# Optimization experiments

Hardware: AMD Instinct MI355X
Metric: run time of the kernel (lower is better)

The kernel has to match this reference:

```python
import jax, jax.numpy as jnp
import numpy as np

B, T, D, M = 4, 2048, 512, 8  # batch, seq, d(=d_out), n_head
LN_EPS = 1e-5


def setup_inputs() -> dict:
    key = jax.random.key(0)
    k = jax.random.split(key, 6)
    s = 1.0 / np.sqrt(D)
    x = jax.random.normal(k[0], (B, T, D), jnp.float32)
    P = jax.random.normal(k[1], (M, D, D), jnp.float32) * s
    Q = jax.random.normal(k[2], (M, D, D), jnp.float32) * s
    K = jax.random.normal(k[3], (M, D, D), jnp.float32) * s
    Wo = jax.random.normal(k[4], (D, M * D), jnp.float32) * (1.0 / np.sqrt(M * D))  # (d_out, m*d), torch Linear layout
    bo = jax.random.normal(k[5], (D,), jnp.float32) * 0.01
    gamma = jnp.ones((D,), jnp.float32)
    beta = jnp.zeros((D,), jnp.float32)
    return {"x": x, "P": P, "Q": Q, "K": K, "Wo": Wo, "bo": bo, "gamma": gamma, "beta": beta}


def reference(x, P, Q, K, Wo, bo, gamma, beta):
    b, t, d = x.shape
    m = P.shape[0]
    # per-head projections: (B,T,d) x (m,d,d) -> (B,m,T,d)
    QZ = jnp.einsum('btj,mij->bmti', x, Q)
    KZ = jnp.einsum('btj,mij->bmti', x, K)   # have_key_proj=True
    PZ = jnp.einsum('btj,mij->bmti', x, P)   # value-side projection
    # causal softmax attention
    scores = jnp.einsum('bmti,bmsi->bmts', QZ, KZ) / jnp.sqrt(jnp.asarray(d, x.dtype))
    mask = jnp.tril(jnp.ones((t, t), dtype=bool))  # (T,T) causal
    scores = jnp.where(mask, scores, -jnp.inf)
    attn = jax.nn.softmax(scores, axis=-1)
    out = jnp.einsum('bmts,bmsi->bmti', attn, PZ)
    # have_output_proj=True: concat heads then Linear(m*d -> d_out)
    out = out.transpose(0, 2, 1, 3).reshape(b, t, m * d)
    y = out @ Wo.T + bo
    # layer norm of (attn_out + residual)
    h = y + x
    mu = jnp.mean(h, axis=-1, keepdims=True)
    var = jnp.var(h, axis=-1, keepdims=True)
    return (h - mu) / jnp.sqrt(var + LN_EPS) * gamma + beta
```

## Files before the change

### kernel.cpp

```cpp
#include <hip/hip_runtime.h>

typedef unsigned short u16;
typedef __attribute__((ext_vector_type(8))) short bf16x8;
typedef __attribute__((ext_vector_type(8))) unsigned short u16x8;
typedef __attribute__((ext_vector_type(4))) float f32x4;

__device__ __forceinline__ float zz_bf2f(u16 u) {
    unsigned v = ((unsigned)u) << 16;
    return __builtin_bit_cast(float, v);
}
__device__ __forceinline__ u16 zz_f2bf(float f) {
    unsigned u = __builtin_bit_cast(unsigned, f);
    u += 0x7fffu + ((u >> 16) & 1u);
    return (u16)(u >> 16);
}

__device__ __forceinline__ u16x8 zz_ld8c(const void* p, size_t idx, bool isf) {
    if (isf) {
        const float* fp = (const float*)p + idx;
        f32x4 v0 = *(const f32x4*)fp;
        f32x4 v1 = *(const f32x4*)(fp + 4);
        u16x8 o;
#pragma unroll
        for (int t = 0; t < 4; t++) {
            o[t] = zz_f2bf(v0[t]);
            o[4 + t] = zz_f2bf(v1[t]);
        }
        return o;
    }
    return *(const u16x8*)((const u16*)p + idx);
}

struct f8 { float v[8]; };
__device__ __forceinline__ f8 zz_ld8f(const void* p, size_t idx, bool isf) {
    f8 r;
    if (isf) {
        const float* fp = (const float*)p + idx;
        f32x4 a = *(const f32x4*)fp;
        f32x4 b = *(const f32x4*)(fp + 4);
#pragma unroll
        for (int t = 0; t < 4; t++) {
            r.v[t] = a[t];
            r.v[4 + t] = b[t];
        }
    } else {
        const u16* up = (const u16*)p + idx;
#pragma unroll
        for (int t = 0; t < 8; t++) r.v[t] = zz_bf2f(up[t]);
    }
    return r;
}

__device__ __forceinline__ bool zz_isf(const void* x) {
    const u16* xu = (const u16*)x;
    int cnt = 0;
    for (int i = 0; i < 64; i++) {
        float v = zz_bf2f(xu[i]);
        float a = fabsf(v);
        if (!(a <= 1e8f) || (v != 0.f && a < 1e-8f)) cnt++;
    }
    return cnt >= 16;
}

#define MFMA16(a, b, c) __builtin_amdgcn_mfma_f32_16x16x32_bf16((a), (b), (c), 0, 0, 0)

__device__ __forceinline__ void zz_gll16(const u16* g, u16* l) {
    __builtin_amdgcn_global_load_lds((const __attribute__((address_space(1))) unsigned int*)g,
                                     (__attribute__((address_space(3))) unsigned int*)l, 16, 0, 0);
}

__global__ __launch_bounds__(256) void zk25_conv(const void* __restrict__ x, const void* __restrict__ p1,
                                                 const void* __restrict__ p2, const void* __restrict__ p3,
                                                 const void* __restrict__ p4, u16* __restrict__ xc,
                                                 u16* __restrict__ c1, u16* __restrict__ c2,
                                                 u16* __restrict__ c3, u16* __restrict__ c4) {
    const bool isf = zz_isf(x);
    const int t = blockIdx.y;
    const void* src = (t == 0) ? x : (t == 1) ? p1 : (t == 2) ? p2 : (t == 3) ? p3 : p4;
    u16* dst = (t == 0) ? xc : (t == 1) ? c1 : (t == 2) ? c2 : (t == 3) ? c3 : c4;
    const unsigned n = (t == 0) ? 4194304u : 2097152u;
    const unsigned i = (blockIdx.x * 256u + threadIdx.x) * 8u;
    if (i >= n) return;
    *(u16x8*)(dst + i) = zz_ld8c(src, i, isf);
}

__device__ __forceinline__ void zz_gemm128(const u16* __restrict__ A, size_t aOff,
                                           const u16* __restrict__ B, size_t bOff,
                                           int K, int lda, int ldb, int tm, int tn,
                                           u16* As, u16* Bs, f32x4 acc[4][4]) {
    const int tid = threadIdx.x;
    const int lane = tid & 63;
    const int wid = tid >> 6;
    const int wr = wid >> 1, wc = wid & 1;
    const int c15 = lane & 15, g4 = lane >> 4;

    const int rA = tid >> 2;
    const int cA = (tid & 3) << 3;
    const u16* pA0 = A + aOff + (size_t)(tm * 128 + rA) * lda + cA;
    const u16* pA1 = pA0 + (size_t)64 * lda;
    const u16* pB0 = B + bOff + (size_t)(tn * 128 + rA) * ldb + cA;
    const u16* pB1 = pB0 + (size_t)64 * ldb;
    u16* sA0 = As + tid * 8;
    u16* sA1 = sA0 + 64 * 32;
    u16* sB0 = Bs + tid * 8;
    u16* sB1 = sB0 + 64 * 32;

    for (int k0 = 0; k0 < K; k0 += 32) {
        __syncthreads();
        zz_gll16(pA0 + k0, sA0);
        zz_gll16(pA1 + k0, sA1);
        zz_gll16(pB0 + k0, sB0);
        zz_gll16(pB1 + k0, sB1);
        __syncthreads();
        bf16x8 af[4], bfr[4];
#pragma unroll
        for (int mf = 0; mf < 4; mf++)
            af[mf] = *(const bf16x8*)(As + (wr * 64 + mf * 16 + c15) * 32 + g4 * 8);
#pragma unroll
        for (int nf = 0; nf < 4; nf++)
            bfr[nf] = *(const bf16x8*)(Bs + (wc * 64 + nf * 16 + c15) * 32 + g4 * 8);
#pragma unroll
        for (int mf = 0; mf < 4; mf++)
#pragma unroll
            for (int nf = 0; nf < 4; nf++) acc[mf][nf] = MFMA16(af[mf], bfr[nf], acc[mf][nf]);
    }
}

__global__ __launch_bounds__(256) void zk25_proj(const u16* __restrict__ xc, int b, int g0, int G,
                                                 const u16* __restrict__ Qc, const u16* __restrict__ Kc,
                                                 const u16* __restrict__ Pc,
                                                 u16* __restrict__ QZ, u16* __restrict__ KZ,
                                                 u16* __restrict__ Vt) {
    __shared__ u16 As[128 * 32];
    __shared__ u16 Bs[128 * 32];
    const size_t TD = (size_t)2048 * 512;
    const size_t WD = (size_t)512 * 512;
    const int seg = blockIdx.y;
    const int part = seg / G;
    const int g = seg - part * G;
    const int head = g0 + g;
    const size_t xOff = (size_t)b * TD;
    const int bx = blockIdx.x;

    f32x4 acc[4][4];
    const f32x4 zf = {0.f, 0.f, 0.f, 0.f};
#pragma unroll
    for (int i = 0; i < 4; i++)
#pragma unroll
        for (int j = 0; j < 4; j++) acc[i][j] = zf;

    const int lane = threadIdx.x & 63;
    const int wid = threadIdx.x >> 6;
    const int wr = wid >> 1, wc = wid & 1;
    const int c15 = lane & 15, g4 = lane >> 4;

    if (part < 2) {
        const u16* W = (part == 0) ? Qc : Kc;
        u16* C = ((part == 0) ? QZ : KZ) + (size_t)g * TD;
        const int tm = bx >> 2, tn = bx & 3;
        zz_gemm128(xc, xOff, W, (size_t)head * WD, 512, 512, 512, tm, tn, As, Bs, acc);
#pragma unroll
        for (int mf = 0; mf < 4; mf++)
#pragma unroll
            for (int nf = 0; nf < 4; nf++) {
                const int row0 = tm * 128 + wr * 64 + mf * 16 + g4 * 4;
                const int col = tn * 128 + wc * 64 + nf * 16 + c15;
#pragma unroll
                for (int r = 0; r < 4; r++) C[(size_t)(row0 + r) * 512 + col] = zz_f2bf(acc[mf][nf][r]);
            }
    } else {
        u16* C = Vt + (size_t)g * TD;
        const int tm = bx >> 4, tn = bx & 15;
        zz_gemm128(Pc, (size_t)head * WD, xc, xOff, 512, 512, 512, tm, tn, As, Bs, acc);
#pragma unroll
        for (int mf = 0; mf < 4; mf++)
#pragma unroll
            for (int nf = 0; nf < 4; nf++) {
                const int row0 = tm * 128 + wr * 64 + mf * 16 + g4 * 4;
                const int col = tn * 128 + wc * 64 + nf * 16 + c15;
#pragma unroll
                for (int r = 0; r < 4; r++) C[(size_t)(row0 + r) * 2048 + col] = zz_f2bf(acc[mf][nf][r]);
            }
    }
}

__global__ __launch_bounds__(256) void zk25_qk(const u16* __restrict__ QZ, const u16* __restrict__ KZ,
                                               u16* __restrict__ Sp) {
    const int tm = blockIdx.x, tn = blockIdx.y;
    if (tn > tm) return;
    const int g = blockIdx.z;
    __shared__ u16 As[128 * 32];
    __shared__ u16 Bs[128 * 32];
    const size_t TD = (size_t)2048 * 512;

    f32x4 acc[4][4];
    const f32x4 zf = {0.f, 0.f, 0.f, 0.f};
#pragma unroll
    for (int i = 0; i < 4; i++)
#pragma unroll
        for (int j = 0; j < 4; j++) acc[i][j] = zf;

    zz_gemm128(QZ, (size_t)g * TD, KZ, (size_t)g * TD, 512, 512, 512, tm, tn, As, Bs, acc);

    const int lane = threadIdx.x & 63;
    const int wid = threadIdx.x >> 6;
    const int wr = wid >> 1, wc = wid & 1;
    const int c15 = lane & 15, g4 = lane >> 4;
    u16* Sg = Sp + (size_t)g * 2048 * 2048;
#pragma unroll
    for (int mf = 0; mf < 4; mf++)
#pragma unroll
        for (int nf = 0; nf < 4; nf++) {
            const int row0 = tm * 128 + wr * 64 + mf * 16 + g4 * 4;
            const int col = tn * 128 + wc * 64 + nf * 16 + c15;
#pragma unroll
            for (int r = 0; r < 4; r++) Sg[(size_t)(row0 + r) * 2048 + col] = zz_f2bf(acc[mf][nf][r]);
        }
}

__global__ __launch_bounds__(256) void zk25_sm(u16* __restrict__ Sp) {
    const int g = blockIdx.y;
    const int wid = threadIdx.x >> 6, lane = threadIdx.x & 63;
    const int t = blockIdx.x * 4 + wid;
    u16* rowp = Sp + (size_t)g * 2048 * 2048 + (size_t)t * 2048 + lane * 32;
    const float SCL2 = 0.06375826722338107f;
    u16x8 raw[4];
#pragma unroll
    for (int i = 0; i < 4; i++) raw[i] = *(const u16x8*)(rowp + i * 8);
    float v[32];
    float mx = -INFINITY;
#pragma unroll
    for (int i = 0; i < 32; i++) {
        const int s = lane * 32 + i;
        v[i] = (s <= t) ? zz_bf2f(raw[i >> 3][i & 7]) * SCL2 : -INFINITY;
        mx = fmaxf(mx, v[i]);
    }
#pragma unroll
    for (int d = 1; d < 64; d <<= 1) mx = fmaxf(mx, __shfl_xor(mx, d));
    float p[32];
    float sum = 0.f;
#pragma unroll
    for (int i = 0; i < 32; i++) {
        p[i] = exp2f(v[i] - mx);
        sum += p[i];
    }
#pragma unroll
    for (int d = 1; d < 64; d <<= 1) sum += __shfl_xor(sum, d);
    const float inv = 1.f / sum;
#pragma unroll
    for (int i = 0; i < 4; i++) {
        u16x8 o;
#pragma unroll
        for (int j = 0; j < 8; j++) o[j] = zz_f2bf(p[i * 8 + j] * inv);
        *(u16x8*)(rowp + i * 8) = o;
    }
}

__global__ __launch_bounds__(256) void zk25_pv(const u16* __restrict__ Sp, const u16* __restrict__ Vt,
                                               u16* __restrict__ Oc, int g0) {
    __shared__ u16 As[128 * 32];
    __shared__ u16 Bs[128 * 32];
    const int g = blockIdx.y;
    const int bx = blockIdx.x;
    const int tm = bx >> 2, tn = bx & 3;
    const int K = (tm + 1) * 128;
    const size_t TD = (size_t)2048 * 512;

    f32x4 acc[4][4];
    const f32x4 zf = {0.f, 0.f, 0.f, 0.f};
#pragma unroll
    for (int i = 0; i < 4; i++)
#pragma unroll
        for (int j = 0; j < 4; j++) acc[i][j] = zf;

    zz_gemm128(Sp, (size_t)g * 2048 * 2048, Vt, (size_t)g * TD, K, 2048, 2048, tm, tn, As, Bs, acc);

    const int lane = threadIdx.x & 63;
    const int wid = threadIdx.x >> 6;
    const int wr = wid >> 1, wc = wid & 1;
    const int c15 = lane & 15, g4 = lane >> 4;
    u16* Ob = Oc + (size_t)(g0 + g) * 512;
#pragma unroll
    for (int mf = 0; mf < 4; mf++)
#pragma unroll
        for (int nf = 0; nf < 4; nf++) {
            const int row0 = tm * 128 + wr * 64 + mf * 16 + g4 * 4;
            const int col = tn * 128 + wc * 64 + nf * 16 + c15;
#pragma unroll
            for (int r = 0; r < 4; r++) Ob[(size_t)(row0 + r) * 4096 + col] = zz_f2bf(acc[mf][nf][r]);
        }
}

__global__ __launch_bounds__(256) void zk25_oproj(const u16* __restrict__ Oc, const u16* __restrict__ Woc,
                                                  float* __restrict__ y4) {
    __shared__ u16 As[128 * 32];
    __shared__ u16 Bs[128 * 32];
    const int s = blockIdx.y;
    const int bx = blockIdx.x;
    const int tm = bx >> 2, tn = bx & 3;

    f32x4 acc[4][4];
    const f32x4 zf = {0.f, 0.f, 0.f, 0.f};
#pragma unroll
    for (int i = 0; i < 4; i++)
#pragma unroll
        for (int j = 0; j < 4; j++) acc[i][j] = zf;

    zz_gemm128(Oc, (size_t)s * 1024, Woc, (size_t)s * 1024, 1024, 4096, 4096, tm, tn, As, Bs, acc);

    const int lane = threadIdx.x & 63;
    const int wid = threadIdx.x >> 6;
    const int wr = wid >> 1, wc = wid & 1;
    const int c15 = lane & 15, g4 = lane >> 4;
    float* yb = y4 + (size_t)s * 2048 * 512;
#pragma unroll
    for (int mf = 0; mf < 4; mf++)
#pragma unroll
        for (int nf = 0; nf < 4; nf++) {
            const int row0 = tm * 128 + wr * 64 + mf * 16 + g4 * 4;
            const int col = tn * 128 + wc * 64 + nf * 16 + c15;
#pragma unroll
            for (int r = 0; r < 4; r++) yb[(size_t)(row0 + r) * 512 + col] = acc[mf][nf][r];
        }
}

__global__ __launch_bounds__(256) void zk25_ln(const float* __restrict__ y4, const void* __restrict__ x,
                                               int b, const void* __restrict__ bo,
                                               const void* __restrict__ ga, const void* __restrict__ be,
                                               void* __restrict__ outbase) {
    const bool isf = zz_isf(x);
    const int wid = threadIdx.x >> 6, lane = threadIdx.x & 63;
    const int row = blockIdx.x * 4 + wid;
    const size_t grow = (size_t)b * 2048 + row;
    const int d0 = lane * 8;
    f8 xv = zz_ld8f(x, grow * 512 + d0, isf);
    f8 bov = zz_ld8f(bo, d0, isf);
    float h[8];
#pragma unroll
    for (int j = 0; j < 8; j++) h[j] = bov.v[j] + xv.v[j];
#pragma unroll
    for (int s = 0; s < 4; s++) {
        const float* yp = y4 + (size_t)s * 2048 * 512 + (size_t)row * 512 + d0;
        f32x4 a0 = *(const f32x4*)(yp);
        f32x4 a1 = *(const f32x4*)(yp + 4);
#pragma unroll
        for (int j = 0; j < 4; j++) {
            h[j] += a0[j];
            h[4 + j] += a1[j];
        }
    }
    float sum = 0.f, sq = 0.f;
#pragma unroll
    for (int j = 0; j < 8; j++) {
        sum += h[j];
        sq += h[j] * h[j];
    }
#pragma unroll
    for (int d = 1; d < 64; d <<= 1) {
        sum += __shfl_xor(sum, d);
        sq += __shfl_xor(sq, d);
    }
    const float mean = sum * (1.f / 512.f);
    const float var = sq * (1.f / 512.f) - mean * mean;
    const float rstd = rsqrtf(var + 1e-5f);
    f8 gv = zz_ld8f(ga, d0, isf);
    f8 bv = zz_ld8f(be, d0, isf);
    const size_t o = grow * 512 + d0;
    if (isf) {
        float* op = (float*)outbase + o;
#pragma unroll
        for (int j = 0; j < 8; j++) op[j] = (h[j] - mean) * rstd * gv.v[j] + bv.v[j];
    } else {
        u16* op = (u16*)outbase + o;
#pragma unroll
        for (int j = 0; j < 8; j++) op[j] = zz_f2bf((h[j] - mean) * rstd * gv.v[j] + bv.v[j]);
    }
}

__global__ __launch_bounds__(256) void zk25_band(float* __restrict__ out, float val) {
    const size_t gid = (size_t)blockIdx.x * 256 + threadIdx.x;
    float* p = out + gid * 8;
#pragma unroll
    for (int j = 0; j < 8; j++) p[j] = val;
}

extern "C" void kernel_launch(void* const* d_in, const int* in_sizes, int n_in, void* d_out,
                              int out_size, void* d_ws, size_t ws_size, hipStream_t stream) {
    if (n_in != 8 || in_sizes[0] != 4194304 || in_sizes[5] != 512) {
        zk25_band<<<dim3(2048), dim3(256), 0, stream>>>((float*)d_out, 16.0f);
        return;
    }
    const void* x = d_in[0];
    const void* Pw = d_in[1];
    const void* Qw = d_in[2];
    const void* Kw = d_in[3];
    const void* Wo = d_in[4];
    const void* bo = d_in[5];
    const void* ga = d_in[6];
    const void* be = d_in[7];

    const size_t TD = (size_t)2048 * 512;

    const size_t convB = 2 * (256 + 4194304 + 4 * 2097152);
    auto need = [&](int g) -> size_t {
        return convB + (size_t)g * (3 * TD * 2 + (size_t)2048 * 2048 * 2) + (size_t)2048 * 4096 * 2;
    };
    int G = 2;
    if (ws_size >= need(8)) G = 8;
    else if (ws_size >= need(4)) G = 4;

    u16* xc = (u16*)d_ws + 256;
    u16* Pc = xc + 4194304;
    u16* Qc = Pc + 2097152;
    u16* Kc = Qc + 2097152;
    u16* Woc = Kc + 2097152;
    u16* QZ = Woc + 2097152;
    u16* KZ = QZ + (size_t)G * TD;
    u16* Vt = KZ + (size_t)G * TD;
    u16* Sp = Vt + (size_t)G * TD;
    u16* Oc = Sp + (size_t)G * 2048 * 2048;
    float* y4 = (float*)Sp;

    zk25_conv<<<dim3(2048, 5), dim3(256), 0, stream>>>(x, Pw, Qw, Kw, Wo, xc, Pc, Qc, Kc, Woc);

    for (int b = 0; b < 4; b++) {
        for (int g0 = 0; g0 < 8; g0 += G) {
            zk25_proj<<<dim3(64, 3 * G), dim3(256), 0, stream>>>(xc, b, g0, G, Qc, Kc, Pc, QZ, KZ, Vt);
            zk25_qk<<<dim3(16, 16, G), dim3(256), 0, stream>>>(QZ, KZ, Sp);
            zk25_sm<<<dim3(512, G), dim3(256), 0, stream>>>(Sp);
            zk25_pv<<<dim3(64, G), dim3(256), 0, stream>>>(Sp, Vt, Oc, g0);
        }
        zk25_oproj<<<dim3(64, 4), dim3(256), 0, stream>>>(Oc, Woc, y4);
        zk25_ln<<<dim3(512), dim3(256), 0, stream>>>(y4, x, b, bo, ga, be, d_out);
    }
}
```

Measured before the change: 836.2 us.

## Batch all-head projections into one wide GEMM, compact causal QK grid, skip masked softmax IO

Projection now runs once per batch as a single GEMM over all 8 heads' concatenated weights (x times a 512x4096 matrix), replacing several small per-group launches and improving weight and x reuse. The QK kernel launches only the 136 lower-triangular tiles, mapped through a triangular index, instead of a 16x16 grid where most upper blocks exit early. Softmax skips reading fully masked upper chunks and writes only up to the tile boundary that PV reads. Workspace layout changes so QZ, KZ and Vt hold all heads, which raises memory use and forces G to be at least 4.

```diff
diff --git a/kernel.cpp b/kernel.cpp
--- a/kernel.cpp
+++ b/kernel.cpp
@@ -69,7 +69,7 @@
                                      (__attribute__((address_space(3))) unsigned int*)l, 16, 0, 0);
 }
 
-__global__ __launch_bounds__(256) void zk25_conv(const void* __restrict__ x, const void* __restrict__ p1,
+__global__ __launch_bounds__(256) void zk26_conv(const void* __restrict__ x, const void* __restrict__ p1,
                                                  const void* __restrict__ p2, const void* __restrict__ p3,
                                                  const void* __restrict__ p4, u16* __restrict__ xc,
                                                  u16* __restrict__ c1, u16* __restrict__ c2,
@@ -126,7 +126,7 @@
     }
 }
 
-__global__ __launch_bounds__(256) void zk25_proj(const u16* __restrict__ xc, int b, int g0, int G,
+__global__ __launch_bounds__(256) void zk26_proj(const u16* __restrict__ xc, int b,
                                                  const u16* __restrict__ Qc, const u16* __restrict__ Kc,
                                                  const u16* __restrict__ Pc,
                                                  u16* __restrict__ QZ, u16* __restrict__ KZ,
@@ -134,11 +134,7 @@
     __shared__ u16 As[128 * 32];
     __shared__ u16 Bs[128 * 32];
     const size_t TD = (size_t)2048 * 512;
-    const size_t WD = (size_t)512 * 512;
-    const int seg = blockIdx.y;
-    const int part = seg / G;
-    const int g = seg - part * G;
-    const int head = g0 + g;
+    const int part = blockIdx.y;
     const size_t xOff = (size_t)b * TD;
     const int bx = blockIdx.x;
 
@@ -156,9 +152,9 @@
 
     if (part < 2) {
         const u16* W = (part == 0) ? Qc : Kc;
-        u16* C = ((part == 0) ? QZ : KZ) + (size_t)g * TD;
-        const int tm = bx >> 2, tn = bx & 3;
-        zz_gemm128(xc, xOff, W, (size_t)head * WD, 512, 512, 512, tm, tn, As, Bs, acc);
+        u16* C = (part == 0) ? QZ : KZ;
+        const int tm = bx >> 5, tn = bx & 31;
+        zz_gemm128(xc, xOff, W, 0, 512, 512, 512, tm, tn, As, Bs, acc);
 #pragma unroll
         for (int mf = 0; mf < 4; mf++)
 #pragma unroll
@@ -166,12 +162,11 @@
                 const int row0 = tm * 128 + wr * 64 + mf * 16 + g4 * 4;
                 const int col = tn * 128 + wc * 64 + nf * 16 + c15;
 #pragma unroll
-                for (int r = 0; r < 4; r++) C[(size_t)(row0 + r) * 512 + col] = zz_f2bf(acc[mf][nf][r]);
+                for (int r = 0; r < 4; r++) C[(size_t)(row0 + r) * 4096 + col] = zz_f2bf(acc[mf][nf][r]);
             }
     } else {
-        u16* C = Vt + (size_t)g * TD;
         const int tm = bx >> 4, tn = bx & 15;
-        zz_gemm128(Pc, (size_t)head * WD, xc, xOff, 512, 512, 512, tm, tn, As, Bs, acc);
+        zz_gemm128(Pc, 0, xc, xOff, 512, 512, 512, tm, tn, As, Bs, acc);
 #pragma unroll
         for (int mf = 0; mf < 4; mf++)
 #pragma unroll
@@ -179,19 +174,23 @@
                 const int row0 = tm * 128 + wr * 64 + mf * 16 + g4 * 4;
                 const int col = tn * 128 + wc * 64 + nf * 16 + c15;
 #pragma unroll
-                for (int r = 0; r < 4; r++) C[(size_t)(row0 + r) * 2048 + col] = zz_f2bf(acc[mf][nf][r]);
+                for (int r = 0; r < 4; r++) Vt[(size_t)(row0 + r) * 2048 + col] = zz_f2bf(acc[mf][nf][r]);
             }
     }
 }
 
-__global__ __launch_bounds__(256) void zk25_qk(const u16* __restrict__ QZ, const u16* __restrict__ KZ,
-                                               u16* __restrict__ Sp) {
-    const int tm = blockIdx.x, tn = blockIdx.y;
-    if (tn > tm) return;
-    const int g = blockIdx.z;
+__global__ __launch_bounds__(256) void zk26_qk(const u16* __restrict__ QZ, const u16* __restrict__ KZ,
+                                               u16* __restrict__ Sp, int g0) {
+    const int g = blockIdx.y;
+    const int head = g0 + g;
+    int bx = blockIdx.x;
+    int tm = (int)((sqrtf(8.f * (float)bx + 1.f) - 1.f) * 0.5f);
+    while ((tm + 1) * (tm + 2) / 2 <= bx) tm++;
+    while (tm * (tm + 1) / 2 > bx) tm--;
+    const int tn = bx - tm * (tm + 1) / 2;
+
     __shared__ u16 As[128 * 32];
     __shared__ u16 Bs[128 * 32];
-    const size_t TD = (size_t)2048 * 512;
 
     f32x4 acc[4][4];
     const f32x4 zf = {0.f, 0.f, 0.f, 0.f};
@@ -200,7 +199,7 @@
 #pragma unroll
         for (int j = 0; j < 4; j++) acc[i][j] = zf;
 
-    zz_gemm128(QZ, (size_t)g * TD, KZ, (size_t)g * TD, 512, 512, 512, tm, tn, As, Bs, acc);
+    zz_gemm128(QZ, (size_t)head * 512, KZ, (size_t)head * 512, 512, 4096, 4096, tm, tn, As, Bs, acc);
 
     const int lane = threadIdx.x & 63;
     const int wid = threadIdx.x >> 6;
@@ -218,15 +217,18 @@
         }
 }
 
-__global__ __launch_bounds__(256) void zk25_sm(u16* __restrict__ Sp) {
+__global__ __launch_bounds__(256) void zk26_sm(u16* __restrict__ Sp) {
     const int g = blockIdx.y;
     const int wid = threadIdx.x >> 6, lane = threadIdx.x & 63;
     const int t = blockIdx.x * 4 + wid;
     u16* rowp = Sp + (size_t)g * 2048 * 2048 + (size_t)t * 2048 + lane * 32;
     const float SCL2 = 0.06375826722338107f;
-    u16x8 raw[4];
-#pragma unroll
-    for (int i = 0; i < 4; i++) raw[i] = *(const u16x8*)(rowp + i * 8);
+    const bool doRead = (lane * 32 <= t);
+    u16x8 raw[4] = {};
+    if (doRead) {
+#pragma unroll
+        for (int i = 0; i < 4; i++) raw[i] = *(const u16x8*)(rowp + i * 8);
+    }
     float v[32];
     float mx = -INFINITY;
 #pragma unroll
@@ -247,16 +249,18 @@
 #pragma unroll
     for (int d = 1; d < 64; d <<= 1) sum += __shfl_xor(sum, d);
     const float inv = 1.f / sum;
-#pragma unroll
-    for (int i = 0; i < 4; i++) {
-        u16x8 o;
-#pragma unroll
-        for (int j = 0; j < 8; j++) o[j] = zz_f2bf(p[i * 8 + j] * inv);
-        *(u16x8*)(rowp + i * 8) = o;
-    }
-}
-
-__global__ __launch_bounds__(256) void zk25_pv(const u16* __restrict__ Sp, const u16* __restrict__ Vt,
+    if (lane * 32 <= (t | 127)) {
+#pragma unroll
+        for (int i = 0; i < 4; i++) {
+            u16x8 o;
+#pragma unroll
+            for (int j = 0; j < 8; j++) o[j] = zz_f2bf(p[i * 8 + j] * inv);
+            *(u16x8*)(rowp + i * 8) = o;
+        }
+    }
+}
+
+__global__ __launch_bounds__(256) void zk26_pv(const u16* __restrict__ Sp, const u16* __restrict__ Vt,
                                                u16* __restrict__ Oc, int g0) {
     __shared__ u16 As[128 * 32];
     __shared__ u16 Bs[128 * 32];
@@ -264,7 +268,6 @@
     const int bx = blockIdx.x;
     const int tm = bx >> 2, tn = bx & 3;
     const int K = (tm + 1) * 128;
-    const size_t TD = (size_t)2048 * 512;
 
     f32x4 acc[4][4];
     const f32x4 zf = {0.f, 0.f, 0.f, 0.f};
@@ -273,7 +276,8 @@
 #pragma unroll
         for (int j = 0; j < 4; j++) acc[i][j] = zf;
 
-    zz_gemm128(Sp, (size_t)g * 2048 * 2048, Vt, (size_t)g * TD, K, 2048, 2048, tm, tn, As, Bs, acc);
+    zz_gemm128(Sp, (size_t)g * 2048 * 2048, Vt, (size_t)(g0 + g) * 512 * 2048, K, 2048, 2048, tm, tn,
+               As, Bs, acc);
 
     const int lane = threadIdx.x & 63;
     const int wid = threadIdx.x >> 6;
@@ -291,7 +295,7 @@
         }
 }
 
-__global__ __launch_bounds__(256) void zk25_oproj(const u16* __restrict__ Oc, const u16* __restrict__ Woc,
+__global__ __launch_bounds__(256) void zk26_oproj(const u16* __restrict__ Oc, const u16* __restrict__ Woc,
                                                   float* __restrict__ y4) {
     __shared__ u16 As[128 * 32];
     __shared__ u16 Bs[128 * 32];
@@ -324,7 +328,7 @@
         }
 }
 
-__global__ __launch_bounds__(256) void zk25_ln(const float* __restrict__ y4, const void* __restrict__ x,
+__global__ __launch_bounds__(256) void zk26_ln(const float* __restrict__ y4, const void* __restrict__ x,
                                                int b, const void* __restrict__ bo,
                                                const void* __restrict__ ga, const void* __restrict__ be,
                                                void* __restrict__ outbase) {
@@ -377,7 +381,7 @@
     }
 }
 
-__global__ __launch_bounds__(256) void zk25_band(float* __restrict__ out, float val) {
+__global__ __launch_bounds__(256) void zk26_band(float* __restrict__ out, float val) {
     const size_t gid = (size_t)blockIdx.x * 256 + threadIdx.x;
     float* p = out + gid * 8;
 #pragma unroll
@@ -387,7 +391,7 @@
 extern "C" void kernel_launch(void* const* d_in, const int* in_sizes, int n_in, void* d_out,
                               int out_size, void* d_ws, size_t ws_size, hipStream_t stream) {
     if (n_in != 8 || in_sizes[0] != 4194304 || in_sizes[5] != 512) {
-        zk25_band<<<dim3(2048), dim3(256), 0, stream>>>((float*)d_out, 16.0f);
+        zk26_band<<<dim3(2048), dim3(256), 0, stream>>>((float*)d_out, 16.0f);
         return;
     }
     const void* x = d_in[0];
@@ -399,15 +403,13 @@
     const void* ga = d_in[6];
     const void* be = d_in[7];
 
-    const size_t TD = (size_t)2048 * 512;
-
     const size_t convB = 2 * (256 + 4194304 + 4 * 2097152);
     auto need = [&](int g) -> size_t {
-        return convB + (size_t)g * (3 * TD * 2 + (size_t)2048 * 2048 * 2) + (size_t)2048 * 4096 * 2;
+        return convB + 3 * (size_t)2048 * 4096 * 2 + (size_t)g * 2048 * 2048 * 2 +
+               (size_t)2048 * 4096 * 2;
     };
-    int G = 2;
+    int G = 4;
     if (ws_size >= need(8)) G = 8;
-    else if (ws_size >= need(4)) G = 4;
 
     u16* xc = (u16*)d_ws + 256;
     u16* Pc = xc + 4194304;
@@ -415,22 +417,22 @@
     u16* Kc = Qc + 2097152;
     u16* Woc = Kc + 2097152;
     u16* QZ = Woc + 2097152;
-    u16* KZ = QZ + (size_t)G * TD;
-    u16* Vt = KZ + (size_t)G * TD;
-    u16* Sp = Vt + (size_t)G * TD;
+    u16* KZ = QZ + (size_t)2048 * 4096;
+    u16* Vt = KZ + (size_t)2048 * 4096;
+    u16* Sp = Vt + (size_t)4096 * 2048;
     u16* Oc = Sp + (size_t)G * 2048 * 2048;
     float* y4 = (float*)Sp;
 
-    zk25_conv<<<dim3(2048, 5), dim3(256), 0, stream>>>(x, Pw, Qw, Kw, Wo, xc, Pc, Qc, Kc, Woc);
+    zk26_conv<<<dim3(2048, 5), dim3(256), 0, stream>>>(x, Pw, Qw, Kw, Wo, xc, Pc, Qc, Kc, Woc);
 
     for (int b = 0; b < 4; b++) {
+        zk26_proj<<<dim3(512, 3), dim3(256), 0, stream>>>(xc, b, Qc, Kc, Pc, QZ, KZ, Vt);
         for (int g0 = 0; g0 < 8; g0 += G) {
-            zk25_proj<<<dim3(64, 3 * G), dim3(256), 0, stream>>>(xc, b, g0, G, Qc, Kc, Pc, QZ, KZ, Vt);
-            zk25_qk<<<dim3(16, 16, G), dim3(256), 0, stream>>>(QZ, KZ, Sp);
-            zk25_sm<<<dim3(512, G), dim3(256), 0, stream>>>(Sp);
-            zk25_pv<<<dim3(64, G), dim3(256), 0, stream>>>(Sp, Vt, Oc, g0);
-        }
-        zk25_oproj<<<dim3(64, 4), dim3(256), 0, stream>>>(Oc, Woc, y4);
-        zk25_ln<<<dim3(512), dim3(256), 0, stream>>>(y4, x, b, bo, ga, be, d_out);
-    }
-}
+            zk26_qk<<<dim3(136, G), dim3(256), 0, stream>>>(QZ, KZ, Sp, g0);
+            zk26_sm<<<dim3(512, G), dim3(256), 0, stream>>>(Sp);
+            zk26_pv<<<dim3(64, G), dim3(256), 0, stream>>>(Sp, Vt, Oc, g0);
+        }
+        zk26_oproj<<<dim3(64, 4), dim3(256), 0, stream>>>(Oc, Woc, y4);
+        zk26_ln<<<dim3(512), dim3(256), 0, stream>>>(y4, x, b, bo, ga, be, d_out);
+    }
+}
```

Result: faster. 775.7 us (-7.2%).
